# Optimization experiments

Hardware: AMD Instinct MI355X
Metric: run time of the kernel (lower is better)

## Reference

```python
import jax, jax.numpy as jnp
import numpy as np

D_MODEL = 1024
NUM_HEADS = 16
D_K = D_MODEL // NUM_HEADS


def setup_inputs() -> dict:
    key = jax.random.key(0)
    ks = jax.random.split(key, 10)
    s = 1.0 / np.sqrt(D_MODEL)  # ~ torch Linear init scale
    inp = {
        "x": jax.random.normal(ks[0], (2, 2048, D_MODEL), dtype=jnp.float32),
        "Wq": jax.random.uniform(ks[1], (D_MODEL, D_MODEL), jnp.float32, -s, s),
        "bq": jax.random.uniform(ks[2], (D_MODEL,), jnp.float32, -s, s),
        "Wk": jax.random.uniform(ks[3], (D_MODEL, D_MODEL), jnp.float32, -s, s),
        "bk": jax.random.uniform(ks[4], (D_MODEL,), jnp.float32, -s, s),
        "Wv": jax.random.uniform(ks[5], (D_MODEL, D_MODEL), jnp.float32, -s, s),
        "bv": jax.random.uniform(ks[6], (D_MODEL,), jnp.float32, -s, s),
        "Wo": jax.random.uniform(ks[7], (D_MODEL, D_MODEL), jnp.float32, -s, s),
        "bo": jax.random.uniform(ks[8], (D_MODEL,), jnp.float32, -s, s),
        "ln_gamma": jnp.ones((D_MODEL,), jnp.float32),
        "ln_beta": jnp.zeros((D_MODEL,), jnp.float32),
    }
    return inp


def reference(x, Wq, bq, Wk, bk, Wv, bv, Wo, bo, ln_gamma, ln_beta):
    B, S, D = x.shape
    residual = x
    # LayerNorm (eps=1e-5 as torch default)
    mu = jnp.mean(x, axis=-1, keepdims=True)
    var = jnp.mean(jnp.square(x - mu), axis=-1, keepdims=True)
    xn = (x - mu) * jax.lax.rsqrt(var + 1e-5) * ln_gamma + ln_beta
    # QKV projections (torch Linear: y = x @ W^T + b) -> (B, H, S, d_k)
    def proj(W, b):
        return (xn @ W.T + b).reshape(B, S, NUM_HEADS, D_K).transpose(0, 2, 1, 3)
    Q, K, V = proj(Wq, bq), proj(Wk, bk), proj(Wv, bv)
    scores = jnp.einsum("bhqd,bhkd->bhqk", Q, K) / np.sqrt(D_K).astype(np.float32)
    attn = jax.nn.softmax(scores, axis=-1)  # (B, H, S, S); dropout is no-op (eval)
    context = jnp.einsum("bhqk,bhkd->bhqd", attn, V)
    context = context.transpose(0, 2, 1, 3).reshape(B, S, D)
    out = context @ Wo.T + bo
    return out + residual, attn.mean(axis=1)
```

## Files before the change

### kernel.cpp

```cpp
#include <hip/hip_runtime.h>
#include <stdint.h>
#include <stddef.h>

#define DEV static __device__ __forceinline__

typedef float f32x4 __attribute__((ext_vector_type(4)));
typedef float f32x16 __attribute__((ext_vector_type(16)));
typedef unsigned u32x4 __attribute__((ext_vector_type(4)));
typedef __bf16 bf16x8 __attribute__((ext_vector_type(8)));

DEV short f2bf(float f) {
  union { float f; unsigned u; } a; a.f = f;
  unsigned r = a.u + 0x7fffu + ((a.u >> 16) & 1u);
  return (short)(r >> 16);
}

DEV void gld_lds16(const void* g, void* lds) {
  __builtin_amdgcn_global_load_lds(
      (__attribute__((address_space(1))) void*)(void*)g,
      (__attribute__((address_space(3))) void*)lds, 16, 0, 0);
}

DEV f32x4 MFMA(bf16x8 a, bf16x8 b, f32x4 c) {
  return __builtin_amdgcn_mfma_f32_16x16x32_bf16(a, b, c, 0, 0, 0);
}
DEV f32x16 MFMA32(bf16x8 a, bf16x8 b, f32x16 c) {
  return __builtin_amdgcn_mfma_f32_32x32x16_bf16(a, b, c, 0, 0, 0);
}

DEV float ex2(float x) { return __builtin_amdgcn_exp2f(x); }

DEV unsigned cvtpk(float lo, float hi) {
  unsigned r;
  asm("v_cvt_pk_bf16_f32 %0, %1, %2" : "=v"(r) : "v"(lo), "v"(hi));
  return r;
}

DEV float xhalf_max(float v) {
  float a = v, b = v;
  asm volatile("v_permlane32_swap_b32 %0, %1" : "+v"(a), "+v"(b));
  return fmaxf(a, b);
}
DEV float xhalf_sum(float v) {
  float a = v, b = v;
  asm volatile("v_permlane32_swap_b32 %0, %1" : "+v"(a), "+v"(b));
  return a + b;
}

#define LOG2E 1.4426950408889634f


__global__ __launch_bounds__(256) void k_cvtw(const float* __restrict__ w0,
                                              const float* __restrict__ w1,
                                              const float* __restrict__ w2,
                                              const float* __restrict__ w3,
                                              short* __restrict__ dst) {
  int i = blockIdx.x * 256 + threadIdx.x;
  int sel = i >> 18;
  const float* src = sel == 0 ? w0 : sel == 1 ? w1 : sel == 2 ? w2 : w3;
  int off = (i & 0x3ffff) * 4;
  float4 v = *(const float4*)(src + off);
  short4 o4; o4.x = f2bf(v.x); o4.y = f2bf(v.y); o4.z = f2bf(v.z); o4.w = f2bf(v.w);
  *(short4*)(dst + (size_t)i * 4) = o4;
}

__global__ __launch_bounds__(256) void k_ln(const float* __restrict__ x,
                                            const float* __restrict__ g,
                                            const float* __restrict__ be,
                                            short* __restrict__ xn) {
  int row = blockIdx.x;
  int t = threadIdx.x;
  const float4* xr = (const float4*)(x + (size_t)row * 1024);
  float4 v = xr[t];
  float s = v.x + v.y + v.z + v.w;
  float ss = v.x * v.x + v.y * v.y + v.z * v.z + v.w * v.w;
#pragma unroll
  for (int o = 32; o; o >>= 1) { s += __shfl_down(s, o); ss += __shfl_down(ss, o); }
  __shared__ float ps[4], pss[4];
  int w = t >> 6, lane = t & 63;
  if (lane == 0) { ps[w] = s; pss[w] = ss; }
  __syncthreads();
  float st = ps[0] + ps[1] + ps[2] + ps[3];
  float sst = pss[0] + pss[1] + pss[2] + pss[3];
  float mean = st * (1.0f / 1024.0f);
  float var = sst * (1.0f / 1024.0f) - mean * mean;
  float rstd = rsqrtf(var + 1e-5f);
  float4 gv = ((const float4*)g)[t];
  float4 bv = ((const float4*)be)[t];
  short4 o4;
  o4.x = f2bf((v.x - mean) * rstd * gv.x + bv.x);
  o4.y = f2bf((v.y - mean) * rstd * gv.y + bv.y);
  o4.z = f2bf((v.z - mean) * rstd * gv.z + bv.z);
  o4.w = f2bf((v.w - mean) * rstd * gv.w + bv.w);
  ((short4*)(xn + (size_t)row * 1024))[t] = o4;
}

__global__ __launch_bounds__(256) void k_gemm_qkv(
    const short* __restrict__ xn, const short* __restrict__ wbf,
    const float* __restrict__ bq, const float* __restrict__ bk,
    const float* __restrict__ bv, short* __restrict__ q_ws,
    short* __restrict__ k_ws, short* __restrict__ v_ws) {
  __shared__ __align__(16) short at[128 * 32];
  __shared__ __align__(16) short bt[128 * 32];
  int t = threadIdx.x, lane = t & 63, w = t >> 6;
  int wr = w >> 1, wc = w & 1;
  int z = blockIdx.z;
  int row0 = blockIdx.y * 128, col0 = blockIdx.x * 128;
  const short* A = xn + (size_t)row0 * 1024;
  const short* Bw = wbf + (size_t)z * (1024 * 1024) + (size_t)col0 * 1024;
  f32x4 acc[4][4];
#pragma unroll
  for (int m = 0; m < 4; m++)
#pragma unroll
    for (int n = 0; n < 4; n++) acc[m][n] = (f32x4)0.0f;

  for (int k0 = 0; k0 < 1024; k0 += 32) {
#pragma unroll
    for (int i = 0; i < 2; i++) {
      int c = t + i * 256;
      int r = c >> 2, cc = (c & 3) * 8;
      gld_lds16(A + (size_t)r * 1024 + k0 + cc, &at[c * 8]);
      gld_lds16(Bw + (size_t)r * 1024 + k0 + cc, &bt[c * 8]);
    }
    __syncthreads();
    bf16x8 af[4], bfr[4];
#pragma unroll
    for (int m = 0; m < 4; m++)
      af[m] = *(const bf16x8*)&at[(wr * 64 + m * 16 + (lane & 15)) * 32 + (lane >> 4) * 8];
#pragma unroll
    for (int n = 0; n < 4; n++)
      bfr[n] = *(const bf16x8*)&bt[(wc * 64 + n * 16 + (lane & 15)) * 32 + (lane >> 4) * 8];
#pragma unroll
    for (int m = 0; m < 4; m++)
#pragma unroll
      for (int n = 0; n < 4; n++) acc[m][n] = MFMA(af[m], bfr[n], acc[m][n]);
    __syncthreads();
  }
  const float* bias = z == 0 ? bq : z == 1 ? bk : bv;
  short* dst = z == 0 ? q_ws : z == 1 ? k_ws : v_ws;
  float scal = z == 0 ? (0.125f * LOG2E) : 1.0f;
#pragma unroll
  for (int m = 0; m < 4; m++)
#pragma unroll
    for (int n = 0; n < 4; n++)
#pragma unroll
      for (int r = 0; r < 4; r++) {
        int grow = row0 + wr * 64 + m * 16 + (lane >> 4) * 4 + r;
        int gcol = col0 + wc * 64 + n * 16 + (lane & 15);
        float val = (acc[m][n][r] + bias[gcol]) * scal;
        int bb = grow >> 11, s = grow & 2047, h = gcol >> 6, d = gcol & 63;
        dst[(((size_t)bb * 16 + h) * 2048 + s) * 64 + d] = f2bf(val);
      }
}

__global__ __launch_bounds__(256) void k_trv(const short* __restrict__ v_ws,
                                             short* __restrict__ vt_ws) {
  __shared__ short tile[64][65];
  int bh = blockIdx.y, s0 = blockIdx.x * 64;
  const short* src = v_ws + ((size_t)bh * 2048 + s0) * 64;
  int t = threadIdx.x;
#pragma unroll
  for (int i = 0; i < 4; i++) {
    int c = t + i * 256;
    int r = c >> 4, d4 = (c & 15) * 4;
    short4 v4 = *(const short4*)&src[r * 64 + d4];
    tile[d4 + 0][r] = v4.x; tile[d4 + 1][r] = v4.y;
    tile[d4 + 2][r] = v4.z; tile[d4 + 3][r] = v4.w;
  }
  __syncthreads();
#pragma unroll
  for (int i = 0; i < 4; i++) {
    int c = t + i * 256;
    int d = c >> 4, r4 = (c & 15) * 4;
    short4 o4;
    o4.x = tile[d][r4 + 0]; o4.y = tile[d][r4 + 1];
    o4.z = tile[d][r4 + 2]; o4.w = tile[d][r4 + 3];
    *(short4*)&vt_ws[((size_t)bh * 64 + d) * 2048 + s0 + r4] = o4;
  }
}

__global__ __launch_bounds__(256) void k_attn1(
    const short* __restrict__ q_ws, const short* __restrict__ k_ws,
    const short* __restrict__ vt_ws, short* __restrict__ o_ws,
    float* __restrict__ m_ws, float* __restrict__ l_ws) {
  __shared__ __align__(16) short k_lds[2][64 * 64];
  __shared__ __align__(16) short vt_lds[2][64 * 64];
  int t = threadIdx.x, lane = t & 63, w = t >> 6;
  int hi = lane >> 5, l31 = lane & 31;
  int qt = blockIdx.x, hd = blockIdx.y, b = blockIdx.z;
  int bh = b * 16 + hd;
  int q0 = qt * 128;
  const short* qb = q_ws + (size_t)bh * (2048 * 64);
  const short* kb = k_ws + (size_t)bh * (2048 * 64);
  const short* vtb = vt_ws + (size_t)bh * (64 * 2048);
  int qg = q0 + w * 32 + l31;

  bf16x8 qf[4];
#pragma unroll
  for (int d4 = 0; d4 < 4; d4++)
    qf[d4] = *(const bf16x8*)&qb[(size_t)qg * 64 + d4 * 16 + hi * 8];
  asm volatile("s_waitcnt vmcnt(0)" ::: "memory");

#define STG1(kt0, buf)                                                          \
  {                                                                             \
    _Pragma("unroll")                                                           \
    for (int i_ = 0; i_ < 2; i_++) {                                            \
      int c_ = t + i_ * 256;                                                    \
      int r_ = c_ >> 3, j_ = (c_ & 7) ^ (r_ & 7);                               \
      gld_lds16(kb + (size_t)((kt0) + r_) * 64 + j_ * 8, &k_lds[buf][c_ * 8]);  \
    }                                                                           \
    _Pragma("unroll")                                                           \
    for (int i_ = 0; i_ < 2; i_++) {                                            \
      int c_ = t + i_ * 256;                                                    \
      int r_ = c_ >> 3, j_ = (c_ & 7) ^ (r_ & 7);                               \
      gld_lds16(vtb + (size_t)r_ * 2048 + (kt0) + j_ * 8, &vt_lds[buf][c_ * 8]);\
    }                                                                           \
  }

  STG1(0, 0);

  f32x16 Oacc[2];
#pragma unroll
  for (int i = 0; i < 16; i++) { Oacc[0][i] = 0.0f; Oacc[1][i] = 0.0f; }
  float mrun = -1e30f, lrun = 0.0f;

  int cur = 0;
  for (int it = 0; it < 32; ++it) {
    int ktn = (it < 31 ? it + 1 : it) * 64;
    STG1(ktn, cur ^ 1);
    asm volatile("s_waitcnt vmcnt(4)" ::: "memory");
    __builtin_amdgcn_s_barrier();

    const short* kl = k_lds[cur];
    const short* vl = vt_lds[cur];

    f32x16 S0 = (f32x16)0.0f, S1 = (f32x16)0.0f;
#pragma unroll
    for (int d4 = 0; d4 < 4; d4++) {
      int row0 = l31;
      bf16x8 kf0 = *(const bf16x8*)&kl[row0 * 64 + (((d4 * 2 + hi) ^ (row0 & 7)) * 8)];
      int row1 = 32 + l31;
      bf16x8 kf1 = *(const bf16x8*)&kl[row1 * 64 + (((d4 * 2 + hi) ^ (row1 & 7)) * 8)];
      S0 = MFMA32(kf0, qf[d4], S0);
      S1 = MFMA32(kf1, qf[d4], S1);
    }

    float mt;
    {
      float a[8];
#pragma unroll
      for (int i = 0; i < 8; i++) a[i] = fmaxf(S0[i], S0[i + 8]);
#pragma unroll
      for (int i = 0; i < 8; i++) a[i] = fmaxf(a[i], fmaxf(S1[i], S1[i + 8]));
      float b0 = fmaxf(fmaxf(a[0], a[1]), fmaxf(a[2], a[3]));
      float b1 = fmaxf(fmaxf(a[4], a[5]), fmaxf(a[6], a[7]));
      mt = xhalf_max(fmaxf(b0, b1));
    }
    if (!__all(mt - mrun <= 8.0f)) {
      float mn = fmaxf(mrun, mt);
      float sc_ = ex2(mrun - mn);
      lrun *= sc_;
#pragma unroll
      for (int i = 0; i < 16; i++) { Oacc[0][i] *= sc_; Oacc[1][i] *= sc_; }
      mrun = mn;
    }
    float rs0 = 0.0f, rs1 = 0.0f;
#pragma unroll
    for (int i = 0; i < 16; i++) {
      float p0 = ex2(S0[i] - mrun);
      float p1 = ex2(S1[i] - mrun);
      S0[i] = p0; S1[i] = p1;
      rs0 += p0; rs1 += p1;
    }
    lrun += xhalf_sum(rs0 + rs1);

    bf16x8 pb[4];
#pragma unroll
    for (int ks = 0; ks < 4; ks++) {
      unsigned wA, wB, wC, wD;
      if (ks == 0) {
        wA = cvtpk(S0[0], S0[1]);  wB = cvtpk(S0[2], S0[3]);
        wC = cvtpk(S0[4], S0[5]);  wD = cvtpk(S0[6], S0[7]);
      } else if (ks == 1) {
        wA = cvtpk(S0[8], S0[9]);  wB = cvtpk(S0[10], S0[11]);
        wC = cvtpk(S0[12], S0[13]); wD = cvtpk(S0[14], S0[15]);
      } else if (ks == 2) {
        wA = cvtpk(S1[0], S1[1]);  wB = cvtpk(S1[2], S1[3]);
        wC = cvtpk(S1[4], S1[5]);  wD = cvtpk(S1[6], S1[7]);
      } else {
        wA = cvtpk(S1[8], S1[9]);  wB = cvtpk(S1[10], S1[11]);
        wC = cvtpk(S1[12], S1[13]); wD = cvtpk(S1[14], S1[15]);
      }
      asm volatile("v_permlane32_swap_b32 %0, %1" : "+v"(wA), "+v"(wC));
      asm volatile("v_permlane32_swap_b32 %0, %1" : "+v"(wB), "+v"(wD));
      u32x4 uu; uu.x = wA; uu.y = wB; uu.z = wC; uu.w = wD;
      pb[ks] = __builtin_bit_cast(bf16x8, uu);
    }

#pragma unroll
    for (int ks = 0; ks < 4; ks++) {
      int row0 = l31;
      bf16x8 vf0 = *(const bf16x8*)&vl[row0 * 64 + (((ks * 2 + hi) ^ (row0 & 7)) * 8)];
      int row1 = 32 + l31;
      bf16x8 vf1 = *(const bf16x8*)&vl[row1 * 64 + (((ks * 2 + hi) ^ (row1 & 7)) * 8)];
      Oacc[0] = MFMA32(vf0, pb[ks], Oacc[0]);
      Oacc[1] = MFMA32(vf1, pb[ks], Oacc[1]);
    }
    __builtin_amdgcn_s_barrier();
    cur ^= 1;
  }
  asm volatile("s_waitcnt vmcnt(0)" ::: "memory");

  float rl = 1.0f / lrun;
  if (lane < 32) {
    m_ws[bh * 2048 + qg] = mrun;
    l_ws[bh * 2048 + qg] = rl;
  }
#pragma unroll
  for (int dt = 0; dt < 2; dt++)
#pragma unroll
    for (int g = 0; g < 4; g++) {
      short4 o4;
      o4.x = f2bf(Oacc[dt][g * 4 + 0] * rl);
      o4.y = f2bf(Oacc[dt][g * 4 + 1] * rl);
      o4.z = f2bf(Oacc[dt][g * 4 + 2] * rl);
      o4.w = f2bf(Oacc[dt][g * 4 + 3] * rl);
      int d = dt * 32 + g * 8 + hi * 4;
      *(short4*)&o_ws[((size_t)(b * 2048 + qg)) * 1024 + hd * 64 + d] = o4;
    }
}

__global__ __launch_bounds__(256, 3) void k_attn2(
    const short* __restrict__ q_ws, const short* __restrict__ k_ws,
    const float* __restrict__ m_ws, const float* __restrict__ l_ws,
    float* __restrict__ out1) {
  __shared__ __align__(16) short q_lds[2][64 * 64];
  __shared__ __align__(16) short k_lds2[2][128 * 64];
  __shared__ __align__(16) float ml_lds[2][2][64];
  int t = threadIdx.x, lane = t & 63, w = t >> 6;
  int k2 = blockIdx.x * 128, q0 = blockIdx.y * 64, b = blockIdx.z;

  f32x4 pacc[8];
#pragma unroll
  for (int n = 0; n < 8; n++) pacc[n] = (f32x4)0.0f;

#define STAGE2(hh, buf)                                                          \
  {                                                                              \
    int bh_ = b * 16 + (hh);                                                     \
    const short* qb_ = q_ws + (size_t)bh_ * (2048 * 64);                         \
    const short* kb_ = k_ws + (size_t)bh_ * (2048 * 64);                         \
    _Pragma("unroll")                                                            \
    for (int i = 0; i < 2; i++) {                                                \
      int c = t + i * 256;                                                       \
      int r = c >> 3, j = (c & 7) ^ (r & 7);                                     \
      gld_lds16(qb_ + (size_t)(q0 + r) * 64 + j * 8, &q_lds[buf][c * 8]);        \
    }                                                                            \
    _Pragma("unroll")                                                            \
    for (int i = 0; i < 4; i++) {                                                \
      int c = t + i * 256;                                                       \
      int r = c >> 3, j = (c & 7) ^ (r & 7);                                     \
      gld_lds16(kb_ + (size_t)(k2 + r) * 64 + j * 8, &k_lds2[buf][c * 8]);       \
    }                                                                            \
    int cc = w * 8 + (t & 63);                                                   \
    if ((t & 63) < 8) {                                                          \
      const float* src_ = cc < 16 ? &m_ws[(size_t)bh_ * 2048 + q0 + cc * 4]      \
                                  : &l_ws[(size_t)bh_ * 2048 + q0 + (cc - 16) * 4]; \
      gld_lds16(src_, &ml_lds[buf][0][cc * 4]);                                  \
    }                                                                            \
  }

  STAGE2(0, 0);
  int cur = 0;
  for (int h = 0; h < 16; ++h) {
    int hn = h < 15 ? h + 1 : 15;
    STAGE2(hn, cur ^ 1);
    asm volatile("s_waitcnt vmcnt(7)" ::: "memory");
    __builtin_amdgcn_s_barrier();

    const short* ql = q_lds[cur];
    const short* kl = k_lds2[cur];
    bf16x8 qf[2];
#pragma unroll
    for (int kf = 0; kf < 2; kf++) {
      int row = w * 16 + (lane & 15);
      qf[kf] = *(const bf16x8*)&ql[row * 64 + (((kf * 4 + (lane >> 4)) ^ (row & 7)) * 8)];
    }
    f32x4 sc[8];
#pragma unroll
    for (int n = 0; n < 8; n++) sc[n] = (f32x4)0.0f;
#pragma unroll
    for (int kf = 0; kf < 2; kf++)
#pragma unroll
      for (int n = 0; n < 8; n++) {
        int row = n * 16 + (lane & 15);
        bf16x8 kfr = *(const bf16x8*)&kl[row * 64 + (((kf * 4 + (lane >> 4)) ^ (row & 7)) * 8)];
        sc[n] = MFMA(qf[kf], kfr, sc[n]);
      }
    f32x4 mh = *(const f32x4*)&ml_lds[cur][0][w * 16 + (lane >> 4) * 4];
    f32x4 lh = *(const f32x4*)&ml_lds[cur][1][w * 16 + (lane >> 4) * 4];
#pragma unroll
    for (int n = 0; n < 8; n++)
#pragma unroll
      for (int r = 0; r < 4; r++)
        pacc[n][r] += ex2(sc[n][r] - mh[r]) * lh[r];
    __builtin_amdgcn_s_barrier();
    cur ^= 1;
  }

#pragma unroll
  for (int n = 0; n < 8; n++)
#pragma unroll
    for (int r = 0; r < 4; r++) {
      int q = q0 + w * 16 + (lane >> 4) * 4 + r;
      int k = k2 + n * 16 + (lane & 15);
      out1[((size_t)b * 2048 + q) * 2048 + k] = pacc[n][r] * 0.0625f;
    }
}

__global__ __launch_bounds__(256) void k_gemm_out(
    const short* __restrict__ o_ws, const short* __restrict__ wo_bf,
    const float* __restrict__ bo, const float* __restrict__ x,
    float* __restrict__ out0) {
  __shared__ __align__(16) short at[128 * 32];
  __shared__ __align__(16) short bt[128 * 32];
  int t = threadIdx.x, lane = t & 63, w = t >> 6;
  int wr = w >> 1, wc = w & 1;
  int row0 = blockIdx.y * 128, col0 = blockIdx.x * 128;
  const short* A = o_ws + (size_t)row0 * 1024;
  const short* Bw = wo_bf + (size_t)col0 * 1024;
  f32x4 acc[4][4];
#pragma unroll
  for (int m = 0; m < 4; m++)
#pragma unroll
    for (int n = 0; n < 4; n++) acc[m][n] = (f32x4)0.0f;

  for (int k0 = 0; k0 < 1024; k0 += 32) {
#pragma unroll
    for (int i = 0; i < 2; i++) {
      int c = t + i * 256;
      int r = c >> 2, cc = (c & 3) * 8;
      gld_lds16(A + (size_t)r * 1024 + k0 + cc, &at[c * 8]);
      gld_lds16(Bw + (size_t)r * 1024 + k0 + cc, &bt[c * 8]);
    }
    __syncthreads();
    bf16x8 af[4], bfr[4];
#pragma unroll
    for (int m = 0; m < 4; m++)
      af[m] = *(const bf16x8*)&at[(wr * 64 + m * 16 + (lane & 15)) * 32 + (lane >> 4) * 8];
#pragma unroll
    for (int n = 0; n < 4; n++)
      bfr[n] = *(const bf16x8*)&bt[(wc * 64 + n * 16 + (lane & 15)) * 32 + (lane >> 4) * 8];
#pragma unroll
    for (int m = 0; m < 4; m++)
#pragma unroll
      for (int n = 0; n < 4; n++) acc[m][n] = MFMA(af[m], bfr[n], acc[m][n]);
    __syncthreads();
  }
#pragma unroll
  for (int m = 0; m < 4; m++)
#pragma unroll
    for (int n = 0; n < 4; n++)
#pragma unroll
      for (int r = 0; r < 4; r++) {
        int grow = row0 + wr * 64 + m * 16 + (lane >> 4) * 4 + r;
        int gcol = col0 + wc * 64 + n * 16 + (lane & 15);
        float val = acc[m][n][r] + bo[gcol] + x[(size_t)grow * 1024 + gcol];
        out0[(size_t)grow * 1024 + gcol] = val;
      }
}

extern "C" void kernel_launch(void* const* d_in, const int* in_sizes, int n_in,
                              void* d_out, int out_size, void* d_ws, size_t ws_size,
                              hipStream_t stream) {
  (void)in_sizes; (void)n_in; (void)out_size; (void)ws_size;
  const float* x   = (const float*)d_in[0];
  const float* Wq  = (const float*)d_in[1];
  const float* bq  = (const float*)d_in[2];
  const float* Wk  = (const float*)d_in[3];
  const float* bk  = (const float*)d_in[4];
  const float* Wv  = (const float*)d_in[5];
  const float* bv  = (const float*)d_in[6];
  const float* Wo  = (const float*)d_in[7];
  const float* bo  = (const float*)d_in[8];
  const float* lng = (const float*)d_in[9];
  const float* lnb = (const float*)d_in[10];
  float* out0 = (float*)d_out;
  float* out1 = out0 + (size_t)2 * 2048 * 1024;

  char* ws = (char*)d_ws;
  short* xn    = (short*)(ws);
  short* q_ws  = (short*)(ws + 8388608);
  short* k_ws  = (short*)(ws + 16777216);
  short* o_ws  = (short*)(ws + 25165824);
  short* vt_ws = (short*)(ws + 33554432);
  short* wbf   = (short*)(ws + 41943040);
  float* m_ws  = (float*)(ws + 50331648);
  float* l_ws  = (float*)(ws + 50593792);

  k_cvtw<<<4096, 256, 0, stream>>>(Wq, Wk, Wv, Wo, wbf);
  k_ln<<<4096, 256, 0, stream>>>(x, lng, lnb, xn);
  k_gemm_qkv<<<dim3(8, 32, 3), 256, 0, stream>>>(xn, wbf, bq, bk, bv, q_ws, k_ws, o_ws);
  k_trv<<<dim3(32, 32), 256, 0, stream>>>(o_ws, vt_ws);
  k_attn1<<<dim3(16, 16, 2), 256, 0, stream>>>(q_ws, k_ws, vt_ws, o_ws, m_ws, l_ws);
  k_attn2<<<dim3(16, 32, 2), 256, 0, stream>>>(q_ws, k_ws, m_ws, l_ws, out1);
  k_gemm_out<<<dim3(8, 32), 256, 0, stream>>>(o_ws, wbf + (size_t)3 * 1024 * 1024, bo, x, out0);
}
```

Measured before the change: 171.3 us.

## Split attention KV range across two blocks and merge partial results

The flash-attention pass k_attn1 now splits the key/value sequence into two halves, doubling the grid from 512 to 1024 blocks. Each block writes an unnormalized-max partial output plus its running max and sum, and a new k_merge kernel combines the two halves into the final context and the softmax stats. The goal is better CU occupancy and shorter per-block loops on a grid that was too small for the chip. The cost is an extra launch and extra global traffic for the partial outputs, and it reuses workspace buffers (xn, v_ws, vt_ws) as scratch. Staging-address computation is also hoisted out of the loop.

```diff
diff --git a/kernel.cpp b/kernel.cpp
--- a/kernel.cpp
+++ b/kernel.cpp
@@ -181,18 +181,19 @@
 
 __global__ __launch_bounds__(256) void k_attn1(
     const short* __restrict__ q_ws, const short* __restrict__ k_ws,
-    const short* __restrict__ vt_ws, short* __restrict__ o_ws,
-    float* __restrict__ m_ws, float* __restrict__ l_ws) {
+    const short* __restrict__ vt_ws, short* __restrict__ o0,
+    short* __restrict__ o1, float* __restrict__ mp, float* __restrict__ lp) {
   __shared__ __align__(16) short k_lds[2][64 * 64];
   __shared__ __align__(16) short vt_lds[2][64 * 64];
   int t = threadIdx.x, lane = t & 63, w = t >> 6;
   int hi = lane >> 5, l31 = lane & 31;
-  int qt = blockIdx.x, hd = blockIdx.y, b = blockIdx.z;
+  int qt = blockIdx.x, hd = blockIdx.y;
+  int b = blockIdx.z >> 1, hf = blockIdx.z & 1;
   int bh = b * 16 + hd;
   int q0 = qt * 128;
   const short* qb = q_ws + (size_t)bh * (2048 * 64);
-  const short* kb = k_ws + (size_t)bh * (2048 * 64);
-  const short* vtb = vt_ws + (size_t)bh * (64 * 2048);
+  const short* kb = k_ws + (size_t)bh * (2048 * 64) + (size_t)hf * (1024 * 64);
+  const short* vtb = vt_ws + (size_t)bh * (64 * 2048) + hf * 1024;
   int qg = q0 + w * 32 + l31;
 
   bf16x8 qf[4];
@@ -201,20 +202,24 @@
     qf[d4] = *(const bf16x8*)&qb[(size_t)qg * 64 + d4 * 16 + hi * 8];
   asm volatile("s_waitcnt vmcnt(0)" ::: "memory");
 
-#define STG1(kt0, buf)                                                          \
-  {                                                                             \
-    _Pragma("unroll")                                                           \
-    for (int i_ = 0; i_ < 2; i_++) {                                            \
-      int c_ = t + i_ * 256;                                                    \
-      int r_ = c_ >> 3, j_ = (c_ & 7) ^ (r_ & 7);                               \
-      gld_lds16(kb + (size_t)((kt0) + r_) * 64 + j_ * 8, &k_lds[buf][c_ * 8]);  \
-    }                                                                           \
-    _Pragma("unroll")                                                           \
-    for (int i_ = 0; i_ < 2; i_++) {                                            \
-      int c_ = t + i_ * 256;                                                    \
-      int r_ = c_ >> 3, j_ = (c_ & 7) ^ (r_ & 7);                               \
-      gld_lds16(vtb + (size_t)r_ * 2048 + (kt0) + j_ * 8, &vt_lds[buf][c_ * 8]);\
-    }                                                                           \
+  const short *kp0, *kp1, *vp0, *vp1;
+  {
+    int c = t, r = c >> 3, j = (c & 7) ^ (r & 7);
+    kp0 = kb + (size_t)r * 64 + j * 8;
+    vp0 = vtb + (size_t)r * 2048 + j * 8;
+  }
+  {
+    int c = t + 256, r = c >> 3, j = (c & 7) ^ (r & 7);
+    kp1 = kb + (size_t)r * 64 + j * 8;
+    vp1 = vtb + (size_t)r * 2048 + j * 8;
+  }
+
+#define STG1(it_, buf)                                      \
+  {                                                         \
+    gld_lds16(kp0 + (it_) * 4096, &k_lds[buf][t * 8]);      \
+    gld_lds16(kp1 + (it_) * 4096, &k_lds[buf][(t + 256) * 8]); \
+    gld_lds16(vp0 + (it_) * 64, &vt_lds[buf][t * 8]);       \
+    gld_lds16(vp1 + (it_) * 64, &vt_lds[buf][(t + 256) * 8]); \
   }
 
   STG1(0, 0);
@@ -225,9 +230,9 @@
   float mrun = -1e30f, lrun = 0.0f;
 
   int cur = 0;
-  for (int it = 0; it < 32; ++it) {
-    int ktn = (it < 31 ? it + 1 : it) * 64;
-    STG1(ktn, cur ^ 1);
+  for (int it = 0; it < 16; ++it) {
+    int itn = it < 15 ? it + 1 : it;
+    STG1(itn, cur ^ 1);
     asm volatile("s_waitcnt vmcnt(4)" ::: "memory");
     __builtin_amdgcn_s_barrier();
 
@@ -249,9 +254,8 @@
     {
       float a[8];
 #pragma unroll
-      for (int i = 0; i < 8; i++) a[i] = fmaxf(S0[i], S0[i + 8]);
-#pragma unroll
-      for (int i = 0; i < 8; i++) a[i] = fmaxf(a[i], fmaxf(S1[i], S1[i + 8]));
+      for (int i = 0; i < 8; i++)
+        a[i] = fmaxf(fmaxf(S0[i], S0[i + 8]), fmaxf(S1[i], S1[i + 8]));
       float b0 = fmaxf(fmaxf(a[0], a[1]), fmaxf(a[2], a[3]));
       float b1 = fmaxf(fmaxf(a[4], a[5]), fmaxf(a[6], a[7]));
       mt = xhalf_max(fmaxf(b0, b1));
@@ -311,11 +315,13 @@
   }
   asm volatile("s_waitcnt vmcnt(0)" ::: "memory");
 
+  int r_ = bh * 2048 + qg;
   float rl = 1.0f / lrun;
   if (lane < 32) {
-    m_ws[bh * 2048 + qg] = mrun;
-    l_ws[bh * 2048 + qg] = rl;
-  }
+    mp[hf * 65536 + r_] = mrun;
+    lp[hf * 65536 + r_] = lrun;
+  }
+  short* op = hf ? o1 : o0;
 #pragma unroll
   for (int dt = 0; dt < 2; dt++)
 #pragma unroll
@@ -326,8 +332,43 @@
       o4.z = f2bf(Oacc[dt][g * 4 + 2] * rl);
       o4.w = f2bf(Oacc[dt][g * 4 + 3] * rl);
       int d = dt * 32 + g * 8 + hi * 4;
-      *(short4*)&o_ws[((size_t)(b * 2048 + qg)) * 1024 + hd * 64 + d] = o4;
-    }
+      *(short4*)&op[(size_t)r_ * 64 + d] = o4;
+    }
+}
+
+__global__ __launch_bounds__(256) void k_merge(
+    const short* __restrict__ o0, const short* __restrict__ o1,
+    const float* __restrict__ mp, const float* __restrict__ lp,
+    short* __restrict__ ofin, float* __restrict__ m_ws,
+    float* __restrict__ l_ws) {
+  int r = blockIdx.x * 256 + threadIdx.x;
+  int bh = r >> 11, q = r & 2047;
+  int b = bh >> 4, hd = bh & 15;
+  float m0 = mp[r], m1 = mp[65536 + r];
+  float l0 = lp[r], l1 = lp[65536 + r];
+  float m = fmaxf(m0, m1);
+  float w0 = ex2(m0 - m) * l0;
+  float w1 = ex2(m1 - m) * l1;
+  float rl = 1.0f / (w0 + w1);
+  float a0 = w0 * rl, a1 = w1 * rl;
+  m_ws[r] = m;
+  l_ws[r] = rl;
+  const bf16x8* p0 = (const bf16x8*)(o0 + (size_t)r * 64);
+  const bf16x8* p1 = (const bf16x8*)(o1 + (size_t)r * 64);
+  short* pf = ofin + ((size_t)(b * 2048 + q)) * 1024 + hd * 64;
+#pragma unroll
+  for (int i = 0; i < 8; i++) {
+    bf16x8 v0 = p0[i], v1 = p1[i];
+    unsigned wd[4];
+#pragma unroll
+    for (int jj = 0; jj < 4; jj++) {
+      float e0 = a0 * (float)v0[jj * 2] + a1 * (float)v1[jj * 2];
+      float e1 = a0 * (float)v0[jj * 2 + 1] + a1 * (float)v1[jj * 2 + 1];
+      wd[jj] = cvtpk(e0, e1);
+    }
+    u32x4 st; st.x = wd[0]; st.y = wd[1]; st.z = wd[2]; st.w = wd[3];
+    *(u32x4*)&pf[i * 8] = st;
+  }
 }
 
 __global__ __launch_bounds__(256, 3) void k_attn2(
@@ -491,17 +532,22 @@
   short* xn    = (short*)(ws);
   short* q_ws  = (short*)(ws + 8388608);
   short* k_ws  = (short*)(ws + 16777216);
-  short* o_ws  = (short*)(ws + 25165824);
+  short* v_ws  = (short*)(ws + 25165824);
   short* vt_ws = (short*)(ws + 33554432);
   short* wbf   = (short*)(ws + 41943040);
-  float* m_ws  = (float*)(ws + 50331648);
-  float* l_ws  = (float*)(ws + 50593792);
+  float* mp    = (float*)(ws + 50331648);
+  float* lp    = (float*)(ws + 50855936);
+  float* m_ws  = (float*)(ws + 51380224);
+  float* l_ws  = (float*)(ws + 51642368);
 
   k_cvtw<<<4096, 256, 0, stream>>>(Wq, Wk, Wv, Wo, wbf);
   k_ln<<<4096, 256, 0, stream>>>(x, lng, lnb, xn);
-  k_gemm_qkv<<<dim3(8, 32, 3), 256, 0, stream>>>(xn, wbf, bq, bk, bv, q_ws, k_ws, o_ws);
-  k_trv<<<dim3(32, 32), 256, 0, stream>>>(o_ws, vt_ws);
-  k_attn1<<<dim3(16, 16, 2), 256, 0, stream>>>(q_ws, k_ws, vt_ws, o_ws, m_ws, l_ws);
+  k_gemm_qkv<<<dim3(8, 32, 3), 256, 0, stream>>>(xn, wbf, bq, bk, bv, q_ws, k_ws, v_ws);
+  k_trv<<<dim3(32, 32), 256, 0, stream>>>(v_ws, vt_ws);
+  k_attn1<<<dim3(16, 16, 4), 256, 0, stream>>>(q_ws, k_ws, vt_ws,
+                                               (short*)xn, (short*)v_ws, mp, lp);
+  k_merge<<<256, 256, 0, stream>>>((const short*)xn, (const short*)v_ws, mp, lp,
+                                   vt_ws, m_ws, l_ws);
   k_attn2<<<dim3(16, 32, 2), 256, 0, stream>>>(q_ws, k_ws, m_ws, l_ws, out1);
-  k_gemm_out<<<dim3(8, 32), 256, 0, stream>>>(o_ws, wbf + (size_t)3 * 1024 * 1024, bo, x, out0);
-}
+  k_gemm_out<<<dim3(8, 32), 256, 0, stream>>>(vt_ws, wbf + (size_t)3 * 1024 * 1024, bo, x, out0);
+}
```

Measured after the change: 182.7 us. 6.7% more time.

## Software-pipeline attention loop: overlap previous PV MFMAs with current QK

Applied to the files above, without the earlier changes.

Restructures the flash-attention main loop so that the P·V MFMAs for tile it-1 are issued right after the Q·K^T MFMAs for tile it. The softmax and bf16 packing of each tile now overlap with matrix-core work, and a final PV step is added after the loop. K and V loads are split and staggered, with V staged one iteration behind K, and precomputed per-thread global pointers replace the per-iteration address math. MFMA sections are wrapped in s_setprio to favour matrix issue. This costs extra live registers for the carried P fragments, which may reduce occupancy.

```diff
diff --git a/kernel.cpp b/kernel.cpp
--- a/kernel.cpp
+++ b/kernel.cpp
@@ -201,39 +201,47 @@
     qf[d4] = *(const bf16x8*)&qb[(size_t)qg * 64 + d4 * 16 + hi * 8];
   asm volatile("s_waitcnt vmcnt(0)" ::: "memory");
 
-#define STG1(kt0, buf)                                                          \
-  {                                                                             \
-    _Pragma("unroll")                                                           \
-    for (int i_ = 0; i_ < 2; i_++) {                                            \
-      int c_ = t + i_ * 256;                                                    \
-      int r_ = c_ >> 3, j_ = (c_ & 7) ^ (r_ & 7);                               \
-      gld_lds16(kb + (size_t)((kt0) + r_) * 64 + j_ * 8, &k_lds[buf][c_ * 8]);  \
-    }                                                                           \
-    _Pragma("unroll")                                                           \
-    for (int i_ = 0; i_ < 2; i_++) {                                            \
-      int c_ = t + i_ * 256;                                                    \
-      int r_ = c_ >> 3, j_ = (c_ & 7) ^ (r_ & 7);                               \
-      gld_lds16(vtb + (size_t)r_ * 2048 + (kt0) + j_ * 8, &vt_lds[buf][c_ * 8]);\
-    }                                                                           \
-  }
-
-  STG1(0, 0);
+  const short *kp0, *kp1, *vp0, *vp1;
+  {
+    int c = t, r = c >> 3, j = (c & 7) ^ (r & 7);
+    kp0 = kb + (size_t)r * 64 + j * 8;
+    vp0 = vtb + (size_t)r * 2048 + j * 8;
+  }
+  {
+    int c = t + 256, r = c >> 3, j = (c & 7) ^ (r & 7);
+    kp1 = kb + (size_t)r * 64 + j * 8;
+    vp1 = vtb + (size_t)r * 2048 + j * 8;
+  }
+
+#define STG_K(kt_, buf)                                     \
+  {                                                         \
+    gld_lds16(kp0 + (kt_) * 4096, &k_lds[buf][t * 8]);      \
+    gld_lds16(kp1 + (kt_) * 4096, &k_lds[buf][(t + 256) * 8]); \
+  }
+#define STG_V(kt_, buf)                                     \
+  {                                                         \
+    gld_lds16(vp0 + (kt_) * 64, &vt_lds[buf][t * 8]);       \
+    gld_lds16(vp1 + (kt_) * 64, &vt_lds[buf][(t + 256) * 8]); \
+  }
+
+  STG_K(0, 0);
 
   f32x16 Oacc[2];
 #pragma unroll
   for (int i = 0; i < 16; i++) { Oacc[0][i] = 0.0f; Oacc[1][i] = 0.0f; }
   float mrun = -1e30f, lrun = 0.0f;
-
-  int cur = 0;
+  bf16x8 pb0, pb1, pb2, pb3;
+
   for (int it = 0; it < 32; ++it) {
-    int ktn = (it < 31 ? it + 1 : it) * 64;
-    STG1(ktn, cur ^ 1);
+    STG_V(it, it & 1);
+    STG_K(it < 31 ? it + 1 : 31, (it + 1) & 1);
     asm volatile("s_waitcnt vmcnt(4)" ::: "memory");
     __builtin_amdgcn_s_barrier();
 
-    const short* kl = k_lds[cur];
-    const short* vl = vt_lds[cur];
-
+    const short* kl = k_lds[it & 1];
+    const short* vl = vt_lds[(it ^ 1) & 1];
+
+    __builtin_amdgcn_s_setprio(1);
     f32x16 S0 = (f32x16)0.0f, S1 = (f32x16)0.0f;
 #pragma unroll
     for (int d4 = 0; d4 < 4; d4++) {
@@ -244,14 +252,26 @@
       S0 = MFMA32(kf0, qf[d4], S0);
       S1 = MFMA32(kf1, qf[d4], S1);
     }
+    if (it) {
+#pragma unroll
+      for (int ks = 0; ks < 4; ks++) {
+        bf16x8 pk = ks == 0 ? pb0 : ks == 1 ? pb1 : ks == 2 ? pb2 : pb3;
+        int row0 = l31;
+        bf16x8 vf0 = *(const bf16x8*)&vl[row0 * 64 + (((ks * 2 + hi) ^ (row0 & 7)) * 8)];
+        int row1 = 32 + l31;
+        bf16x8 vf1 = *(const bf16x8*)&vl[row1 * 64 + (((ks * 2 + hi) ^ (row1 & 7)) * 8)];
+        Oacc[0] = MFMA32(vf0, pk, Oacc[0]);
+        Oacc[1] = MFMA32(vf1, pk, Oacc[1]);
+      }
+    }
+    __builtin_amdgcn_s_setprio(0);
 
     float mt;
     {
       float a[8];
 #pragma unroll
-      for (int i = 0; i < 8; i++) a[i] = fmaxf(S0[i], S0[i + 8]);
-#pragma unroll
-      for (int i = 0; i < 8; i++) a[i] = fmaxf(a[i], fmaxf(S1[i], S1[i + 8]));
+      for (int i = 0; i < 8; i++)
+        a[i] = fmaxf(fmaxf(S0[i], S0[i + 8]), fmaxf(S1[i], S1[i + 8]));
       float b0 = fmaxf(fmaxf(a[0], a[1]), fmaxf(a[2], a[3]));
       float b1 = fmaxf(fmaxf(a[4], a[5]), fmaxf(a[6], a[7]));
       mt = xhalf_max(fmaxf(b0, b1));
@@ -274,42 +294,53 @@
     }
     lrun += xhalf_sum(rs0 + rs1);
 
-    bf16x8 pb[4];
-#pragma unroll
-    for (int ks = 0; ks < 4; ks++) {
+    {
       unsigned wA, wB, wC, wD;
-      if (ks == 0) {
-        wA = cvtpk(S0[0], S0[1]);  wB = cvtpk(S0[2], S0[3]);
-        wC = cvtpk(S0[4], S0[5]);  wD = cvtpk(S0[6], S0[7]);
-      } else if (ks == 1) {
-        wA = cvtpk(S0[8], S0[9]);  wB = cvtpk(S0[10], S0[11]);
-        wC = cvtpk(S0[12], S0[13]); wD = cvtpk(S0[14], S0[15]);
-      } else if (ks == 2) {
-        wA = cvtpk(S1[0], S1[1]);  wB = cvtpk(S1[2], S1[3]);
-        wC = cvtpk(S1[4], S1[5]);  wD = cvtpk(S1[6], S1[7]);
-      } else {
-        wA = cvtpk(S1[8], S1[9]);  wB = cvtpk(S1[10], S1[11]);
-        wC = cvtpk(S1[12], S1[13]); wD = cvtpk(S1[14], S1[15]);
-      }
+      wA = cvtpk(S0[0], S0[1]);  wB = cvtpk(S0[2], S0[3]);
+      wC = cvtpk(S0[4], S0[5]);  wD = cvtpk(S0[6], S0[7]);
       asm volatile("v_permlane32_swap_b32 %0, %1" : "+v"(wA), "+v"(wC));
       asm volatile("v_permlane32_swap_b32 %0, %1" : "+v"(wB), "+v"(wD));
       u32x4 uu; uu.x = wA; uu.y = wB; uu.z = wC; uu.w = wD;
-      pb[ks] = __builtin_bit_cast(bf16x8, uu);
-    }
-
+      pb0 = __builtin_bit_cast(bf16x8, uu);
+      wA = cvtpk(S0[8], S0[9]);  wB = cvtpk(S0[10], S0[11]);
+      wC = cvtpk(S0[12], S0[13]); wD = cvtpk(S0[14], S0[15]);
+      asm volatile("v_permlane32_swap_b32 %0, %1" : "+v"(wA), "+v"(wC));
+      asm volatile("v_permlane32_swap_b32 %0, %1" : "+v"(wB), "+v"(wD));
+      uu.x = wA; uu.y = wB; uu.z = wC; uu.w = wD;
+      pb1 = __builtin_bit_cast(bf16x8, uu);
+      wA = cvtpk(S1[0], S1[1]);  wB = cvtpk(S1[2], S1[3]);
+      wC = cvtpk(S1[4], S1[5]);  wD = cvtpk(S1[6], S1[7]);
+      asm volatile("v_permlane32_swap_b32 %0, %1" : "+v"(wA), "+v"(wC));
+      asm volatile("v_permlane32_swap_b32 %0, %1" : "+v"(wB), "+v"(wD));
+      uu.x = wA; uu.y = wB; uu.z = wC; uu.w = wD;
+      pb2 = __builtin_bit_cast(bf16x8, uu);
+      wA = cvtpk(S1[8], S1[9]);  wB = cvtpk(S1[10], S1[11]);
+      wC = cvtpk(S1[12], S1[13]); wD = cvtpk(S1[14], S1[15]);
+      asm volatile("v_permlane32_swap_b32 %0, %1" : "+v"(wA), "+v"(wC));
+      asm volatile("v_permlane32_swap_b32 %0, %1" : "+v"(wB), "+v"(wD));
+      uu.x = wA; uu.y = wB; uu.z = wC; uu.w = wD;
+      pb3 = __builtin_bit_cast(bf16x8, uu);
+    }
+    __builtin_amdgcn_s_barrier();
+  }
+  asm volatile("s_waitcnt vmcnt(0)" ::: "memory");
+  __builtin_amdgcn_s_barrier();
+
+  {
+    const short* vl = vt_lds[1];
+    __builtin_amdgcn_s_setprio(1);
 #pragma unroll
     for (int ks = 0; ks < 4; ks++) {
+      bf16x8 pk = ks == 0 ? pb0 : ks == 1 ? pb1 : ks == 2 ? pb2 : pb3;
       int row0 = l31;
       bf16x8 vf0 = *(const bf16x8*)&vl[row0 * 64 + (((ks * 2 + hi) ^ (row0 & 7)) * 8)];
       int row1 = 32 + l31;
       bf16x8 vf1 = *(const bf16x8*)&vl[row1 * 64 + (((ks * 2 + hi) ^ (row1 & 7)) * 8)];
-      Oacc[0] = MFMA32(vf0, pb[ks], Oacc[0]);
-      Oacc[1] = MFMA32(vf1, pb[ks], Oacc[1]);
-    }
-    __builtin_amdgcn_s_barrier();
-    cur ^= 1;
-  }
-  asm volatile("s_waitcnt vmcnt(0)" ::: "memory");
+      Oacc[0] = MFMA32(vf0, pk, Oacc[0]);
+      Oacc[1] = MFMA32(vf1, pk, Oacc[1]);
+    }
+    __builtin_amdgcn_s_setprio(0);
+  }
 
   float rl = 1.0f / lrun;
   if (lane < 32) {
```

Result: no change. 168.1 us (-1.8%).
